# Kernel optimization log

Hardware: AMD Instinct MI355X
Metric: run time of the kernel (lower is better)

The kernel has to match this reference:

```python
import jax, jax.numpy as jnp
import numpy as np

TAU = 1.0
TOP_K = 2
TOP_C = 8
EPS = 1e-12


def _stable_softmax(v):
    # matches torch: exp(v - max) / (sum + 1e-12)
    e = jnp.exp(v - jnp.max(v, axis=-1, keepdims=True))
    return e / (jnp.sum(e, axis=-1, keepdims=True) + EPS)


def setup_inputs() -> dict:
    key = jax.random.key(0)
    kx, kw = jax.random.split(key)
    B, D, M = 16384, 2048, 64
    x = jax.random.normal(kx, (B, D), dtype=jnp.float32)
    W = jax.random.normal(kw, (M, D), dtype=jnp.float32) * (1.0 / np.sqrt(D))
    return {"x": x, "W": W}


def reference(x, W):
    # router GEMM: [B, D] x [M, D]^T -> [B, M]
    router_logits = jnp.einsum('bd,md->bm', x, W)
    scaled_logits = router_logits / TAU
    probs = _stable_softmax(scaled_logits)
    # double top-k: first candidates (top_c), then top_k among candidates
    topc_vals, topc_idx = jax.lax.top_k(scaled_logits, TOP_C)   # [B, C]
    topk_vals, topk_pos_in_C = jax.lax.top_k(topc_vals, TOP_K)  # [B, K]
    topk_idx = jnp.take_along_axis(topc_idx, topk_pos_in_C, axis=1)
    topk_weights = _stable_softmax(topk_vals)
    return (topk_idx.astype(jnp.int64), topk_weights, probs, topc_idx.astype(jnp.int64))
```

## Files before the change

kernel.cpp:

```cpp
#include <hip/hip_runtime.h>


typedef __fp16 fp16x2 __attribute__((ext_vector_type(2)));
typedef _Float16 half8_t __attribute__((ext_vector_type(8)));
typedef __attribute__((ext_vector_type(4))) float f32x4;

constexpr int Bq = 16384;
constexpr int Dk = 2048;
constexpr int Me = 64;
constexpr int WAVES = 8;
constexpr int ROWS = 32;
constexpr int KCHUNK = Dk / WAVES;
constexpr int NT = KCHUNK / 32;

constexpr size_t OFF_TOPK_IDX = 0;
constexpr size_t OFF_TOPK_W   = (size_t)Bq * 2;
constexpr size_t OFF_PROBS    = (size_t)Bq * 4;
constexpr size_t OFF_TOPC_IDX = (size_t)Bq * 4 + (size_t)Bq * 64;

__device__ __forceinline__ void split2(const float af[8], half8_t& s0, half8_t& s1) {
  uint4 q0, q1;
  unsigned* p0 = &q0.x; unsigned* p1 = &q1.x;
  #pragma unroll
  for (int p = 0; p < 4; ++p) {
    float a = af[2 * p], b = af[2 * p + 1];
    fp16x2 c0 = __builtin_amdgcn_cvt_pkrtz(a, b);
    float ra = a - (float)c0[0], rb = b - (float)c0[1];
    fp16x2 c1 = __builtin_amdgcn_cvt_pkrtz(ra, rb);
    p0[p] = __builtin_bit_cast(unsigned, c0);
    p1[p] = __builtin_bit_cast(unsigned, c1);
  }
  s0 = __builtin_bit_cast(half8_t, q0);
  s1 = __builtin_bit_cast(half8_t, q1);
}

__global__ void wsplit_kernel(const float* __restrict__ W,
                              unsigned short* __restrict__ w0,
                              unsigned short* __restrict__ w1) {
  int t = blockIdx.x * blockDim.x + threadIdx.x;
  int kt = t >> 8, n = (t >> 6) & 3, L = t & 63;
  int e  = n * 16 + (L & 15);
  int kb = kt * 32 + ((L >> 4) << 3);
  const float* src = W + (size_t)e * Dk + kb;
  float4 a = *reinterpret_cast<const float4*>(src);
  float4 b = *reinterpret_cast<const float4*>(src + 4);
  float af[8] = {a.x, a.y, a.z, a.w, b.x, b.y, b.z, b.w};
  half8_t s0, s1;
  split2(af, s0, s1);
  *reinterpret_cast<half8_t*>(w0 + (size_t)t * 8) = s0;
  *reinterpret_cast<half8_t*>(w1 + (size_t)t * 8) = s1;
}

__global__ __launch_bounds__(512, 2)
void gating_mfma(const float* __restrict__ x,
                 const unsigned short* __restrict__ w0,
                 const unsigned short* __restrict__ w1,
                 float* __restrict__ out) {
  __shared__ __align__(16) char smem[WAVES * ROWS * 36 * 4];
  typedef float XaT[ROWS][36];
  XaT* xa = reinterpret_cast<XaT*>(smem);
  typedef float PartT[ROWS][68];
  PartT* part = reinterpret_cast<PartT*>(smem);

  const int tid  = threadIdx.x;
  const int wv   = tid >> 6;
  const int L    = tid & 63;
  const int lidx = L & 15;
  const int kgrp = L >> 4;
  const int rowBase = blockIdx.x * ROWS;
  const int kBase = wv * KCHUNK;

  const int srow = L >> 3;
  const int sc4  = (L & 7) << 2;
  const float* xg0 = x + (size_t)(rowBase +      srow) * Dk + kBase + sc4;
  const float* xg1 = x + (size_t)(rowBase +  8 + srow) * Dk + kBase + sc4;
  const float* xg2 = x + (size_t)(rowBase + 16 + srow) * Dk + kBase + sc4;
  const float* xg3 = x + (size_t)(rowBase + 24 + srow) * Dk + kBase + sc4;

  const size_t bbase = (size_t)kBase * 64 + (size_t)L * 8;

  f32x4 acc[2][4];
  #pragma unroll
  for (int rg = 0; rg < 2; ++rg)
    #pragma unroll
    for (int n = 0; n < 4; ++n) acc[rg][n] = (f32x4){0.f, 0.f, 0.f, 0.f};

  *reinterpret_cast<float4*>(&xa[wv][     srow][sc4]) = *reinterpret_cast<const float4*>(xg0);
  *reinterpret_cast<float4*>(&xa[wv][ 8 + srow][sc4]) = *reinterpret_cast<const float4*>(xg1);
  *reinterpret_cast<float4*>(&xa[wv][16 + srow][sc4]) = *reinterpret_cast<const float4*>(xg2);
  *reinterpret_cast<float4*>(&xa[wv][24 + srow][sc4]) = *reinterpret_cast<const float4*>(xg3);

  #pragma unroll 1
  for (int kt = 0; kt < NT; ++kt) {
    float4 aLo0 = *reinterpret_cast<const float4*>(&xa[wv][     lidx][kgrp * 8]);
    float4 aHi0 = *reinterpret_cast<const float4*>(&xa[wv][     lidx][kgrp * 8 + 4]);
    float4 aLo1 = *reinterpret_cast<const float4*>(&xa[wv][16 + lidx][kgrp * 8]);
    float4 aHi1 = *reinterpret_cast<const float4*>(&xa[wv][16 + lidx][kgrp * 8 + 4]);

    float4 h0, h1, h2, h3;
    if (kt < NT - 1) {
      h0 = *reinterpret_cast<const float4*>(xg0 + (kt + 1) * 32);
      h1 = *reinterpret_cast<const float4*>(xg1 + (kt + 1) * 32);
      h2 = *reinterpret_cast<const float4*>(xg2 + (kt + 1) * 32);
      h3 = *reinterpret_cast<const float4*>(xg3 + (kt + 1) * 32);
    }

    const size_t to = bbase + (size_t)kt * 2048;

    half8_t b0[4];
    #pragma unroll
    for (int n = 0; n < 4; ++n) b0[n] = *reinterpret_cast<const half8_t*>(w0 + to + n * 512);

    float af0[8] = {aLo0.x, aLo0.y, aLo0.z, aLo0.w, aHi0.x, aHi0.y, aHi0.z, aHi0.w};
    float af1[8] = {aLo1.x, aLo1.y, aLo1.z, aLo1.w, aHi1.x, aHi1.y, aHi1.z, aHi1.w};
    half8_t xs00, xs10, xs01, xs11;
    split2(af0, xs00, xs10);
    split2(af1, xs01, xs11);

    half8_t b1[4];
    #pragma unroll
    for (int n = 0; n < 4; ++n) b1[n] = *reinterpret_cast<const half8_t*>(w1 + to + n * 512);

    #pragma unroll
    for (int n = 0; n < 4; ++n) acc[0][n] = __builtin_amdgcn_mfma_f32_16x16x32_f16(xs00, b0[n], acc[0][n], 0, 0, 0);
    #pragma unroll
    for (int n = 0; n < 4; ++n) acc[1][n] = __builtin_amdgcn_mfma_f32_16x16x32_f16(xs01, b0[n], acc[1][n], 0, 0, 0);
    #pragma unroll
    for (int n = 0; n < 4; ++n) acc[0][n] = __builtin_amdgcn_mfma_f32_16x16x32_f16(xs10, b0[n], acc[0][n], 0, 0, 0);
    #pragma unroll
    for (int n = 0; n < 4; ++n) acc[1][n] = __builtin_amdgcn_mfma_f32_16x16x32_f16(xs11, b0[n], acc[1][n], 0, 0, 0);

    #pragma unroll
    for (int n = 0; n < 4; ++n) acc[0][n] = __builtin_amdgcn_mfma_f32_16x16x32_f16(xs00, b1[n], acc[0][n], 0, 0, 0);
    #pragma unroll
    for (int n = 0; n < 4; ++n) acc[1][n] = __builtin_amdgcn_mfma_f32_16x16x32_f16(xs01, b1[n], acc[1][n], 0, 0, 0);

    if (kt < NT - 1) {
      *reinterpret_cast<float4*>(&xa[wv][     srow][sc4]) = h0;
      *reinterpret_cast<float4*>(&xa[wv][ 8 + srow][sc4]) = h1;
      *reinterpret_cast<float4*>(&xa[wv][16 + srow][sc4]) = h2;
      *reinterpret_cast<float4*>(&xa[wv][24 + srow][sc4]) = h3;
    }
  }

  __syncthreads();
  if (wv >= 4) {
    #pragma unroll
    for (int rg = 0; rg < 2; ++rg)
      #pragma unroll
      for (int n = 0; n < 4; ++n)
        #pragma unroll
        for (int r = 0; r < 4; ++r)
          part[wv - 4][rg * 16 + kgrp * 4 + r][n * 16 + lidx] = acc[rg][n][r];
  }
  __syncthreads();
  if (wv < 4) {
    #pragma unroll
    for (int rg = 0; rg < 2; ++rg)
      #pragma unroll
      for (int n = 0; n < 4; ++n)
        #pragma unroll
        for (int r = 0; r < 4; ++r) {
          float s = acc[rg][n][r] + part[wv][rg * 16 + kgrp * 4 + r][n * 16 + lidx];
          part[wv][rg * 16 + kgrp * 4 + r][n * 16 + lidx] = s;
        }
  }
  __syncthreads();

  const int row = tid >> 4;
  const int g   = tid & 15;
  const int c4  = g * 4;
  const size_t grow = (size_t)rowBase + row;

  float4 v = {0.f, 0.f, 0.f, 0.f};
  #pragma unroll
  for (int p = 0; p < 4; ++p) {
    float4 t = *reinterpret_cast<const float4*>(&part[p][row][c4]);
    v.x += t.x; v.y += t.y; v.z += t.z; v.w += t.w;
  }
  float pv[4] = {v.x, v.y, v.z, v.w};

  float mx = fmaxf(fmaxf(pv[0], pv[1]), fmaxf(pv[2], pv[3]));
  #pragma unroll
  for (int m = 1; m < 16; m <<= 1) mx = fmaxf(mx, __shfl_xor(mx, m));
  float e[4], sum = 0.f;
  #pragma unroll
  for (int j = 0; j < 4; ++j) { e[j] = expf(pv[j] - mx); sum += e[j]; }
  #pragma unroll
  for (int m = 1; m < 16; m <<= 1) sum += __shfl_xor(sum, m);
  const float inv = 1.f / (sum + 1e-12f);
  float4 pw = {e[0] * inv, e[1] * inv, e[2] * inv, e[3] * inv};
  *reinterpret_cast<float4*>(out + OFF_PROBS + grow * 64 + c4) = pw;

  unsigned taken = 0;
  int bidx0 = 0, bidx1 = 0;
  float tv0 = 0.f, tv1 = 0.f;
  #pragma unroll 1
  for (int rank = 0; rank < 8; ++rank) {
    float best = -3.4e38f;
    int bl = -1;
    #pragma unroll
    for (int j = 0; j < 4; ++j)
      if (!((taken >> j) & 1u) && pv[j] > best) { best = pv[j]; bl = j; }
    int bidx = (bl >= 0) ? (c4 + bl) : (1 << 30);
    #pragma unroll
    for (int m = 1; m < 16; m <<= 1) {
      float ov = __shfl_xor(best, m);
      int   oi = __shfl_xor(bidx, m);
      if (ov > best || (ov == best && oi < bidx)) { best = ov; bidx = oi; }
    }
    if (bidx >= c4 && bidx < c4 + 4) taken |= 1u << (bidx - c4);
    if (g == 0) out[OFF_TOPC_IDX + grow * 8 + rank] = (float)bidx;
    if (rank == 0) { tv0 = best; bidx0 = bidx; }
    if (rank == 1) { tv1 = best; bidx1 = bidx; }
  }

  if (g == 0) {
    out[OFF_TOPK_IDX + grow * 2 + 0] = (float)bidx0;
    out[OFF_TOPK_IDX + grow * 2 + 1] = (float)bidx1;
    const float e1  = expf(tv1 - tv0);
    const float den = 1.f + e1 + 1e-12f;
    out[OFF_TOPK_W + grow * 2 + 0] = 1.f / den;
    out[OFF_TOPK_W + grow * 2 + 1] = e1 / den;
  }
}

extern "C" void kernel_launch(void* const* d_in, const int* in_sizes, int n_in,
                              void* d_out, int out_size, void* d_ws, size_t ws_size,
                              hipStream_t stream) {
  const float* x = (const float*)d_in[0];
  const float* W = (const float*)d_in[1];
  float* out = (float*)d_out;

  unsigned short* w0 = (unsigned short*)d_ws;
  unsigned short* w1 = w0 + (size_t)Me * Dk;

  hipLaunchKernelGGL(wsplit_kernel, dim3((Me * Dk / 8) / 256), dim3(256), 0, stream, W, w0, w1);
  hipLaunchKernelGGL(gating_mfma, dim3(Bq / ROWS), dim3(512), 0, stream, x, w0, w1, out);
}
```

Measured before the change: 41.80 us.

## Stage x tiles via direct global-to-LDS loads with swizzled double buffer

Replaces the register-staged prefetch of x (global load into registers, then LDS store) with `__builtin_amdgcn_global_load_lds` into a per-wave double-buffered LDS tile. The tile uses an XOR column swizzle instead of padding to avoid bank conflicts. The W fragment loads are hoisted ahead of the stage call. The cross-wave K reduction becomes a single pass where all 8 waves write partials and the epilogue sums 8 slices, replacing the two-phase 4+4 scheme. This is meant to cut VGPR pressure and instruction overhead on the streaming x path and to drop one barrier. The risks are missing waits on the async LDS writes before they are read, and bank conflicts from the now unpadded 64-wide partial buffer.

New measurement: 42.28 us. About the same (+1.1%).

```diff
diff --git a/kernel.cpp b/kernel.cpp
--- a/kernel.cpp
+++ b/kernel.cpp
@@ -56,10 +56,8 @@
                  const unsigned short* __restrict__ w0,
                  const unsigned short* __restrict__ w1,
                  float* __restrict__ out) {
-  __shared__ __align__(16) char smem[WAVES * ROWS * 36 * 4];
-  typedef float XaT[ROWS][36];
-  XaT* xa = reinterpret_cast<XaT*>(smem);
-  typedef float PartT[ROWS][68];
+  __shared__ __align__(16) float smem[2 * WAVES * ROWS * 32];
+  typedef float PartT[ROWS][64];
   PartT* part = reinterpret_cast<PartT*>(smem);
 
   const int tid  = threadIdx.x;
@@ -71,11 +69,18 @@
   const int kBase = wv * KCHUNK;
 
   const int srow = L >> 3;
-  const int sc4  = (L & 7) << 2;
-  const float* xg0 = x + (size_t)(rowBase +      srow) * Dk + kBase + sc4;
-  const float* xg1 = x + (size_t)(rowBase +  8 + srow) * Dk + kBase + sc4;
-  const float* xg2 = x + (size_t)(rowBase + 16 + srow) * Dk + kBase + sc4;
-  const float* xg3 = x + (size_t)(rowBase + 24 + srow) * Dk + kBase + sc4;
+  const int scol = ((L & 7) ^ (srow & 7)) << 2;
+  const float* xg0 = x + (size_t)(rowBase +      srow) * Dk + kBase + scol;
+  const float* xg1 = x + (size_t)(rowBase +  8 + srow) * Dk + kBase + scol;
+  const float* xg2 = x + (size_t)(rowBase + 16 + srow) * Dk + kBase + scol;
+  const float* xg3 = x + (size_t)(rowBase + 24 + srow) * Dk + kBase + scol;
+
+  float* tile0 = smem + (size_t)wv * (ROWS * 32);
+  float* tile1 = smem + (size_t)(WAVES + wv) * (ROWS * 32);
+
+  const int s7 = lidx & 7;
+  const int u0 = ((2 * kgrp)     ^ s7) << 2;
+  const int u1 = ((2 * kgrp + 1) ^ s7) << 2;
 
   const size_t bbase = (size_t)kBase * 64 + (size_t)L * 8;
 
@@ -85,31 +90,41 @@
     #pragma unroll
     for (int n = 0; n < 4; ++n) acc[rg][n] = (f32x4){0.f, 0.f, 0.f, 0.f};
 
-  *reinterpret_cast<float4*>(&xa[wv][     srow][sc4]) = *reinterpret_cast<const float4*>(xg0);
-  *reinterpret_cast<float4*>(&xa[wv][ 8 + srow][sc4]) = *reinterpret_cast<const float4*>(xg1);
-  *reinterpret_cast<float4*>(&xa[wv][16 + srow][sc4]) = *reinterpret_cast<const float4*>(xg2);
-  *reinterpret_cast<float4*>(&xa[wv][24 + srow][sc4]) = *reinterpret_cast<const float4*>(xg3);
+  auto stage = [&](float* lb, int kt_) {
+    const int o = kt_ * 32;
+    __builtin_amdgcn_global_load_lds(
+        (const __attribute__((address_space(1))) void*)(xg0 + o),
+        (__attribute__((address_space(3))) void*)(lb),             16, 0, 0);
+    __builtin_amdgcn_global_load_lds(
+        (const __attribute__((address_space(1))) void*)(xg1 + o),
+        (__attribute__((address_space(3))) void*)(lb + 8 * 32),    16, 0, 0);
+    __builtin_amdgcn_global_load_lds(
+        (const __attribute__((address_space(1))) void*)(xg2 + o),
+        (__attribute__((address_space(3))) void*)(lb + 16 * 32),   16, 0, 0);
+    __builtin_amdgcn_global_load_lds(
+        (const __attribute__((address_space(1))) void*)(xg3 + o),
+        (__attribute__((address_space(3))) void*)(lb + 24 * 32),   16, 0, 0);
+  };
+
+  stage(tile0, 0);
 
   #pragma unroll 1
   for (int kt = 0; kt < NT; ++kt) {
-    float4 aLo0 = *reinterpret_cast<const float4*>(&xa[wv][     lidx][kgrp * 8]);
-    float4 aHi0 = *reinterpret_cast<const float4*>(&xa[wv][     lidx][kgrp * 8 + 4]);
-    float4 aLo1 = *reinterpret_cast<const float4*>(&xa[wv][16 + lidx][kgrp * 8]);
-    float4 aHi1 = *reinterpret_cast<const float4*>(&xa[wv][16 + lidx][kgrp * 8 + 4]);
-
-    float4 h0, h1, h2, h3;
-    if (kt < NT - 1) {
-      h0 = *reinterpret_cast<const float4*>(xg0 + (kt + 1) * 32);
-      h1 = *reinterpret_cast<const float4*>(xg1 + (kt + 1) * 32);
-      h2 = *reinterpret_cast<const float4*>(xg2 + (kt + 1) * 32);
-      h3 = *reinterpret_cast<const float4*>(xg3 + (kt + 1) * 32);
-    }
-
     const size_t to = bbase + (size_t)kt * 2048;
 
-    half8_t b0[4];
+    half8_t b0[4], b1[4];
     #pragma unroll
     for (int n = 0; n < 4; ++n) b0[n] = *reinterpret_cast<const half8_t*>(w0 + to + n * 512);
+    #pragma unroll
+    for (int n = 0; n < 4; ++n) b1[n] = *reinterpret_cast<const half8_t*>(w1 + to + n * 512);
+
+    if (kt + 1 < NT) stage(((kt + 1) & 1) ? tile1 : tile0, kt + 1);
+
+    float* tb = (kt & 1) ? tile1 : tile0;
+    float4 aLo0 = *reinterpret_cast<const float4*>(tb + (     lidx) * 32 + u0);
+    float4 aHi0 = *reinterpret_cast<const float4*>(tb + (     lidx) * 32 + u1);
+    float4 aLo1 = *reinterpret_cast<const float4*>(tb + (16 + lidx) * 32 + u0);
+    float4 aHi1 = *reinterpret_cast<const float4*>(tb + (16 + lidx) * 32 + u1);
 
     float af0[8] = {aLo0.x, aLo0.y, aLo0.z, aLo0.w, aHi0.x, aHi0.y, aHi0.z, aHi0.w};
     float af1[8] = {aLo1.x, aLo1.y, aLo1.z, aLo1.w, aHi1.x, aHi1.y, aHi1.z, aHi1.w};
@@ -117,10 +132,6 @@
     split2(af0, xs00, xs10);
     split2(af1, xs01, xs11);
 
-    half8_t b1[4];
-    #pragma unroll
-    for (int n = 0; n < 4; ++n) b1[n] = *reinterpret_cast<const half8_t*>(w1 + to + n * 512);
-
     #pragma unroll
     for (int n = 0; n < 4; ++n) acc[0][n] = __builtin_amdgcn_mfma_f32_16x16x32_f16(xs00, b0[n], acc[0][n], 0, 0, 0);
     #pragma unroll
@@ -134,37 +145,17 @@
     for (int n = 0; n < 4; ++n) acc[0][n] = __builtin_amdgcn_mfma_f32_16x16x32_f16(xs00, b1[n], acc[0][n], 0, 0, 0);
     #pragma unroll
     for (int n = 0; n < 4; ++n) acc[1][n] = __builtin_amdgcn_mfma_f32_16x16x32_f16(xs01, b1[n], acc[1][n], 0, 0, 0);
-
-    if (kt < NT - 1) {
-      *reinterpret_cast<float4*>(&xa[wv][     srow][sc4]) = h0;
-      *reinterpret_cast<float4*>(&xa[wv][ 8 + srow][sc4]) = h1;
-      *reinterpret_cast<float4*>(&xa[wv][16 + srow][sc4]) = h2;
-      *reinterpret_cast<float4*>(&xa[wv][24 + srow][sc4]) = h3;
-    }
   }
 
   __syncthreads();
-  if (wv >= 4) {
-    #pragma unroll
-    for (int rg = 0; rg < 2; ++rg)
+
+  #pragma unroll
+  for (int rg = 0; rg < 2; ++rg)
+    #pragma unroll
+    for (int n = 0; n < 4; ++n)
       #pragma unroll
-      for (int n = 0; n < 4; ++n)
-        #pragma unroll
-        for (int r = 0; r < 4; ++r)
-          part[wv - 4][rg * 16 + kgrp * 4 + r][n * 16 + lidx] = acc[rg][n][r];
-  }
-  __syncthreads();
-  if (wv < 4) {
-    #pragma unroll
-    for (int rg = 0; rg < 2; ++rg)
-      #pragma unroll
-      for (int n = 0; n < 4; ++n)
-        #pragma unroll
-        for (int r = 0; r < 4; ++r) {
-          float s = acc[rg][n][r] + part[wv][rg * 16 + kgrp * 4 + r][n * 16 + lidx];
-          part[wv][rg * 16 + kgrp * 4 + r][n * 16 + lidx] = s;
-        }
-  }
+      for (int r = 0; r < 4; ++r)
+        part[wv][rg * 16 + kgrp * 4 + r][n * 16 + lidx] = acc[rg][n][r];
   __syncthreads();
 
   const int row = tid >> 4;
@@ -174,7 +165,7 @@
 
   float4 v = {0.f, 0.f, 0.f, 0.f};
   #pragma unroll
-  for (int p = 0; p < 4; ++p) {
+  for (int p = 0; p < WAVES; ++p) {
     float4 t = *reinterpret_cast<const float4*>(&part[p][row][c4]);
     v.x += t.x; v.y += t.y; v.z += t.z; v.w += t.w;
   }
```

## Split K across blocks and move softmax/top-k into separate finish kernel

Applied to the files above, without the earlier changes.

Each GEMM block now covers 64 rows and half of the K dimension, with waves split as 2 row-halves by 4 K-quarters. Each block writes partial logits to a workspace buffer, and a new finish kernel adds the two halves and then runs the softmax and top-k epilogue. This is meant to halve the W-fragment traffic per row, since each wave's B tiles now serve more rows, and to drop one reduction barrier. In exchange it adds a global round trip for partial logits (about 8 MB written and read) and a third kernel launch.

After: 43.10 us. 1.03x slower.

```diff
diff --git a/kernel.cpp b/kernel.cpp
--- a/kernel.cpp
+++ b/kernel.cpp
@@ -8,9 +8,9 @@
 constexpr int Bq = 16384;
 constexpr int Dk = 2048;
 constexpr int Me = 64;
-constexpr int WAVES = 8;
-constexpr int ROWS = 32;
-constexpr int KCHUNK = Dk / WAVES;
+constexpr int ROWS_BLK = 64;
+constexpr int KHALF = Dk / 2;
+constexpr int KCHUNK = KHALF / 4;
 constexpr int NT = KCHUNK / 32;
 
 constexpr size_t OFF_TOPK_IDX = 0;
@@ -55,27 +55,32 @@
 void gating_mfma(const float* __restrict__ x,
                  const unsigned short* __restrict__ w0,
                  const unsigned short* __restrict__ w1,
-                 float* __restrict__ out) {
-  __shared__ __align__(16) char smem[WAVES * ROWS * 36 * 4];
-  typedef float XaT[ROWS][36];
+                 float* __restrict__ pl) {
+  __shared__ __align__(16) char smem[4 * ROWS_BLK * 68 * 4];
+  typedef float XaT[32][36];
   XaT* xa = reinterpret_cast<XaT*>(smem);
-  typedef float PartT[ROWS][68];
+  typedef float PartT[ROWS_BLK][68];
   PartT* part = reinterpret_cast<PartT*>(smem);
 
   const int tid  = threadIdx.x;
   const int wv   = tid >> 6;
+  const int rh   = wv >> 2;
+  const int kq   = wv & 3;
   const int L    = tid & 63;
   const int lidx = L & 15;
   const int kgrp = L >> 4;
-  const int rowBase = blockIdx.x * ROWS;
-  const int kBase = wv * KCHUNK;
+  const int bx    = blockIdx.x;
+  const int khalf = bx & 1;
+  const int rowBase = (bx >> 1) * ROWS_BLK;
+  const int wrowBase = rowBase + rh * 32;
+  const int kBase = khalf * KHALF + kq * KCHUNK;
 
   const int srow = L >> 3;
   const int sc4  = (L & 7) << 2;
-  const float* xg0 = x + (size_t)(rowBase +      srow) * Dk + kBase + sc4;
-  const float* xg1 = x + (size_t)(rowBase +  8 + srow) * Dk + kBase + sc4;
-  const float* xg2 = x + (size_t)(rowBase + 16 + srow) * Dk + kBase + sc4;
-  const float* xg3 = x + (size_t)(rowBase + 24 + srow) * Dk + kBase + sc4;
+  const float* xg0 = x + (size_t)(wrowBase +      srow) * Dk + kBase + sc4;
+  const float* xg1 = x + (size_t)(wrowBase +  8 + srow) * Dk + kBase + sc4;
+  const float* xg2 = x + (size_t)(wrowBase + 16 + srow) * Dk + kBase + sc4;
+  const float* xg3 = x + (size_t)(wrowBase + 24 + srow) * Dk + kBase + sc4;
 
   const size_t bbase = (size_t)kBase * 64 + (size_t)L * 8;
 
@@ -144,41 +149,44 @@
   }
 
   __syncthreads();
-  if (wv >= 4) {
-    #pragma unroll
-    for (int rg = 0; rg < 2; ++rg)
+  #pragma unroll
+  for (int rg = 0; rg < 2; ++rg)
+    #pragma unroll
+    for (int n = 0; n < 4; ++n)
       #pragma unroll
-      for (int n = 0; n < 4; ++n)
-        #pragma unroll
-        for (int r = 0; r < 4; ++r)
-          part[wv - 4][rg * 16 + kgrp * 4 + r][n * 16 + lidx] = acc[rg][n][r];
-  }
+      for (int r = 0; r < 4; ++r)
+        part[kq][rh * 32 + rg * 16 + kgrp * 4 + r][n * 16 + lidx] = acc[rg][n][r];
   __syncthreads();
-  if (wv < 4) {
-    #pragma unroll
-    for (int rg = 0; rg < 2; ++rg)
-      #pragma unroll
-      for (int n = 0; n < 4; ++n)
-        #pragma unroll
-        for (int r = 0; r < 4; ++r) {
-          float s = acc[rg][n][r] + part[wv][rg * 16 + kgrp * 4 + r][n * 16 + lidx];
-          part[wv][rg * 16 + kgrp * 4 + r][n * 16 + lidx] = s;
-        }
-  }
-  __syncthreads();
-
+
+  const int row = tid >> 3;
+  const int g   = tid & 7;
+  const int c8  = g * 8;
+  const size_t grow = (size_t)rowBase + row;
+
+  float4 va = {0.f, 0.f, 0.f, 0.f}, vb = {0.f, 0.f, 0.f, 0.f};
+  #pragma unroll
+  for (int p = 0; p < 4; ++p) {
+    float4 ta = *reinterpret_cast<const float4*>(&part[p][row][c8]);
+    float4 tb = *reinterpret_cast<const float4*>(&part[p][row][c8 + 4]);
+    va.x += ta.x; va.y += ta.y; va.z += ta.z; va.w += ta.w;
+    vb.x += tb.x; vb.y += tb.y; vb.z += tb.z; vb.w += tb.w;
+  }
+  float* dst = pl + ((size_t)khalf * Bq + grow) * 64 + c8;
+  *reinterpret_cast<float4*>(dst)     = va;
+  *reinterpret_cast<float4*>(dst + 4) = vb;
+}
+
+__global__ __launch_bounds__(256)
+void gating_finish(const float* __restrict__ pl, float* __restrict__ out) {
+  const int tid = threadIdx.x;
   const int row = tid >> 4;
   const int g   = tid & 15;
   const int c4  = g * 4;
-  const size_t grow = (size_t)rowBase + row;
-
-  float4 v = {0.f, 0.f, 0.f, 0.f};
-  #pragma unroll
-  for (int p = 0; p < 4; ++p) {
-    float4 t = *reinterpret_cast<const float4*>(&part[p][row][c4]);
-    v.x += t.x; v.y += t.y; v.z += t.z; v.w += t.w;
-  }
-  float pv[4] = {v.x, v.y, v.z, v.w};
+  const size_t grow = (size_t)blockIdx.x * 16 + row;
+
+  float4 a = *reinterpret_cast<const float4*>(pl + grow * 64 + c4);
+  float4 b = *reinterpret_cast<const float4*>(pl + ((size_t)Bq + grow) * 64 + c4);
+  float pv[4] = {a.x + b.x, a.y + b.y, a.z + b.z, a.w + b.w};
 
   float mx = fmaxf(fmaxf(pv[0], pv[1]), fmaxf(pv[2], pv[3]));
   #pragma unroll
@@ -234,7 +242,9 @@
 
   unsigned short* w0 = (unsigned short*)d_ws;
   unsigned short* w1 = w0 + (size_t)Me * Dk;
+  float* pl = (float*)((char*)d_ws + (size_t)2 * Me * Dk * sizeof(unsigned short));
 
   hipLaunchKernelGGL(wsplit_kernel, dim3((Me * Dk / 8) / 256), dim3(256), 0, stream, W, w0, w1);
-  hipLaunchKernelGGL(gating_mfma, dim3(Bq / ROWS), dim3(512), 0, stream, x, w0, w1, out);
-}
+  hipLaunchKernelGGL(gating_mfma, dim3((Bq / ROWS_BLK) * 2), dim3(512), 0, stream, x, w0, w1, pl);
+  hipLaunchKernelGGL(gating_finish, dim3(Bq / 16), dim3(256), 0, stream, pl, out);
+}
```
